# Optimization experiments

Hardware: AMD Instinct MI355X
Metric: run time of the kernel (lower is better)

The kernel has to match this reference:

```python
import jax, jax.numpy as jnp
import numpy as np

B, S, D = 4, 2048, 1024

def setup_inputs() -> dict:
    key = jax.random.key(0)
    kx, kq, kk, kv = jax.random.split(key, 4)
    scale = 0.02
    return {
        'x': jax.random.normal(kx, (B, S, D), dtype=jnp.float32),
        'wq': jax.random.normal(kq, (D, D), dtype=jnp.float32) * scale,
        'wk': jax.random.normal(kk, (D, D), dtype=jnp.float32) * scale,
        'wv': jax.random.normal(kv, (D, D), dtype=jnp.float32) * scale,
    }

def reference(x, wq, wk, wv):
    # QKV projections (no bias): nn.Linear applies x @ W^T; here wq is already [d_in, d_out]
    q = jnp.einsum('bsd,de->bse', x, wq)
    k = jnp.einsum('bsd,de->bse', x, wk)
    v = jnp.einsum('bsd,de->bse', x, wv)
    d_k = k.shape[-1]
    scores = jnp.einsum('bqd,bkd->bqk', q, k) / jnp.sqrt(jnp.float32(d_k))
    s = x.shape[1]
    causal = jnp.tril(jnp.ones((s, s), dtype=bool))  # True = keep
    scores = jnp.where(causal[None, :, :], scores, -jnp.inf)
    attn = jax.nn.softmax(scores, axis=-1)
    # dropout p=0.0 -> identity
    return jnp.einsum('bqk,bkd->bqd', attn, v)
```

## Files before the change

### kernel.cpp

```cpp
#include <hip/hip_runtime.h>
#include <hip/hip_bf16.h>


typedef __attribute__((ext_vector_type(8))) short bf16x8;
typedef __attribute__((ext_vector_type(4))) float f32x4;

#define GLOAD_LDS16(g, l)                                                     \
    __builtin_amdgcn_global_load_lds(                                         \
        (const __attribute__((address_space(1))) void*)(g),                   \
        (__attribute__((address_space(3))) void*)(l), 16, 0, 0)

__device__ __forceinline__ short f2bf(float f) {
    union { float f; unsigned u; } v; v.f = f;
    unsigned r = v.u + 0x7FFFu + ((v.u >> 16) & 1u);
    return (short)(r >> 16);
}
__device__ __forceinline__ float bf2f(short h) {
    union { unsigned u; float f; } v;
    v.u = ((unsigned)(unsigned short)h) << 16;
    return v.f;
}

__global__ __launch_bounds__(256) void convall(
    const float* __restrict__ x, const float* __restrict__ wq,
    const float* __restrict__ wk, short* __restrict__ xb,
    short* __restrict__ wqb, short* __restrict__ wkb) {
    int i = blockIdx.x * 256 + threadIdx.x;
#pragma unroll
    for (int s = 0; s < 5; ++s) {
        int v = i + s * 524288;
        const float* src;
        short* dst;
        int off;
        if (v < 2097152)      { src = x;  dst = xb;  off = v; }
        else if (v < 2359296) { src = wq; dst = wqb; off = v - 2097152; }
        else                  { src = wk; dst = wkb; off = v - 2359296; }
        float4 w = ((const float4*)src)[off];
        short4 o;
        o.x = f2bf(w.x); o.y = f2bf(w.y); o.z = f2bf(w.z); o.w = f2bf(w.w);
        ((short4*)dst)[off] = o;
    }
}

__global__ __launch_bounds__(256) void wtrans(const float* __restrict__ W,
                                              short* __restrict__ O) {
    int n0 = blockIdx.x * 64, k0 = blockIdx.y * 64;
    __shared__ float tile[64][65];
    int t = threadIdx.x;
#pragma unroll
    for (int i = 0; i < 16; ++i) {
        int idx = t + i * 256;
        int r = idx >> 6, c = idx & 63;
        tile[r][c] = W[(size_t)(k0 + r) * 1024 + n0 + c];
    }
    __syncthreads();
#pragma unroll
    for (int i = 0; i < 16; ++i) {
        int idx = t + i * 256;
        int r = idx >> 6, c = idx & 63;
        O[(size_t)(n0 + r) * 1024 + k0 + c] = f2bf(tile[c][r]);
    }
}

template <int MODE>
__global__ __launch_bounds__(256, 3) void gemm128(
    const short* __restrict__ A0, int lda0, long long sA,
    const short* __restrict__ B0, int ldb0, long long sB,
    void* __restrict__ C0, float scale,
    const short* __restrict__ Av, const short* __restrict__ Bv,
    short* __restrict__ Cv) {

    int m0, n0, z = 0, lda = lda0, ldb = ldb0;
    const short* Ab;
    const short* Bb;
    bool isVT = false;

    {
        const int nblk = gridDim.x;
        const int raw = blockIdx.x;
        int bid = (raw & 7) * (nblk >> 3) + (raw >> 3);
        if (MODE == 5) {
            m0 = (bid >> 3) * 128;
            n0 = (bid & 7) * 128;
            Ab = A0; Bb = B0;
        } else {
            if (bid < 544) {
                z = bid / 136;
                int f = bid - z * 136;
                int mt = (int)((sqrtf(8.f * f + 1.f) - 1.f) * 0.5f);
                if (mt * (mt + 1) / 2 > f) --mt;
                if ((mt + 1) * (mt + 2) / 2 <= f) ++mt;
                int nt_ = f - mt * (mt + 1) / 2;
                m0 = mt * 128; n0 = nt_ * 128;
                Ab = A0 + (size_t)z * sA;
                Bb = B0 + (size_t)z * sB;
            } else {
                isVT = true;
                int v = bid - 544;
                m0 = (v >> 6) * 128;
                n0 = (v & 63) * 128;
                Ab = Av; Bb = Bv; lda = 1024; ldb = 1024;
            }
        }
    }

    const int tid = threadIdx.x;
    const int lane = tid & 63;
    const int wid = tid >> 6;
    const int wm = wid >> 1, wn = wid & 1;

    __shared__ __align__(16) short As[3][4096];
    __shared__ __align__(16) short Bs[3][4096];

    f32x4 acc[4][4] = {};

    const int nt = 32;

    const int srow = tid >> 2;
    const int sl = (tid & 3) ^ ((tid >> 3) & 3);
    const short* Agp = Ab + (size_t)(m0 + srow) * lda + sl * 8;
    const short* Bgp = Bb + (size_t)(n0 + srow) * ldb + sl * 8;

#define SA(kt, bf)                                                            \
    do {                                                                      \
        const int _k = (kt) << 5;                                             \
        GLOAD_LDS16(Agp + _k,                    &As[bf][tid * 8]);           \
        GLOAD_LDS16(Agp + _k + (size_t)64 * lda, &As[bf][2048 + tid * 8]);    \
    } while (0)
#define SB(kt, bf)                                                            \
    do {                                                                      \
        const int _k = (kt) << 5;                                             \
        GLOAD_LDS16(Bgp + _k,                    &Bs[bf][tid * 8]);           \
        GLOAD_LDS16(Bgp + _k + (size_t)64 * ldb, &Bs[bf][2048 + tid * 8]);    \
    } while (0)

    const int r = lane & 15;
    const int g = lane >> 4;

#define LDA4(dst, bf)                                                         \
    _Pragma("unroll") for (int q_ = 0; q_ < 4; ++q_) {                        \
        const int rr = wm * 64 + q_ * 16 + r;                                 \
        dst[q_] = *(const bf16x8*)&As[bf][rr * 32 +                           \
                                          ((g ^ ((rr >> 1) & 3))) * 8];       \
    }
#define LDB4(dst, bf)                                                         \
    _Pragma("unroll") for (int q_ = 0; q_ < 4; ++q_) {                        \
        const int rb = wn * 64 + q_ * 16 + r;                                 \
        dst[q_] = *(const bf16x8*)&Bs[bf][rb * 32 +                           \
                                          ((g ^ ((rb >> 1) & 3))) * 8];       \
    }
#define LGKM0()                                                               \
    asm volatile("s_waitcnt lgkmcnt(0)" ::: "memory");                        \
    __builtin_amdgcn_sched_barrier(0)
#define VMC(n) asm volatile("s_waitcnt vmcnt(" #n ")" ::: "memory")
#define BAR() __builtin_amdgcn_s_barrier()
#define MF(ar, br)                                                            \
    _Pragma("unroll") for (int mi = 0; mi < 4; ++mi)                          \
        _Pragma("unroll") for (int ni = 0; ni < 4; ++ni)                      \
            acc[mi][ni] = __builtin_amdgcn_mfma_f32_16x16x32_bf16(            \
                ar[mi], br[ni], acc[mi][ni], 0, 0, 0);

    SA(0, 0); SB(0, 0);
    SA(1, 1); SB(1, 1);

    int bf = 0;
    int bs = 2;
    for (int t = 0; t < nt; ++t) {
        bf16x8 a[4], b[4];
        if (t + 2 < nt) {
            SA(t + 2, bs); SB(t + 2, bs);
            VMC(8);
        } else if (t + 1 < nt) {
            VMC(4);
        } else {
            VMC(0);
        }
        BAR();
        LDA4(a, bf); LDB4(b, bf);
        LGKM0();
        MF(a, b);
        BAR();
        bf = (bf == 2) ? 0 : bf + 1;
        bs = (bs == 2) ? 0 : bs + 1;
    }

    const int r4 = (lane >> 4) * 4;
#pragma unroll
    for (int mi = 0; mi < 4; ++mi) {
#pragma unroll
        for (int ni = 0; ni < 4; ++ni) {
            int col = n0 + wn * 64 + ni * 16 + r;
#pragma unroll
            for (int i = 0; i < 4; ++i) {
                int rr = m0 + wm * 64 + mi * 16 + r4 + i;
                float v = acc[mi][ni][i];
                if (MODE == 5) {
                    ((short*)C0)[(size_t)rr * 1024 + col] = f2bf(v * scale);
                } else {
                    if (isVT) {
                        Cv[(size_t)(col >> 11) * 2097152 +
                           (size_t)rr * 2048 + (col & 2047)] = f2bf(v);
                    } else if (col <= rr) {
                        ((short*)C0)[(size_t)z * 4194304 +
                                     (size_t)rr * 2048 + col] = f2bf(v);
                    }
                }
            }
        }
    }
#undef SA
#undef SB
#undef LDA4
#undef LDB4
#undef LGKM0
#undef VMC
#undef BAR
#undef MF
}

template <int MODE>
__global__ __launch_bounds__(128, 2) void gemm64(
    const short* __restrict__ A0, int lda, long long sA,
    const short* __restrict__ B0, int ldb, long long sB,
    void* __restrict__ C0, float scale) {

    int m0, n0, z = 0;
    const short* Ab;
    const short* Bb;

    if (MODE == 2) {
        int i = blockIdx.x;
        int j = i & 255;
        int mt = j >> 3;
        z = (j >> 1) & 3;
        m0 = mt * 64;
        n0 = ((j & 1) + (i >> 8) * 2) * 128;
        Ab = A0 + (size_t)z * sA;
        Bb = B0 + (size_t)z * sB;
    } else {
        const int nblk = gridDim.x;
        const int raw = blockIdx.x;
        int bid = (raw & 7) * (nblk >> 3) + (raw >> 3);
        m0 = (bid >> 3) * 64;
        n0 = (bid & 7) * 128;
        Ab = A0; Bb = B0;
    }

    const int tid = threadIdx.x;
    const int lane = tid & 63;
    const int wn = tid >> 6;

    __shared__ __align__(16) short As[3][2048];
    __shared__ __align__(16) short Bs[3][4096];

    f32x4 acc[4][4] = {};

    const int Kend = (MODE == 2) ? (((m0 + 63) | 127) + 1) : 1024;
    const int nt = Kend >> 5;

    const int srow = tid >> 2;
    const int sl = (tid & 3) ^ ((tid >> 3) & 3);
    const short* Agp = Ab + (size_t)(m0 + srow) * lda + sl * 8;
    const short* Bgp = Bb + (size_t)(n0 + srow) * ldb + sl * 8;

#define SA6(kt, bf)                                                           \
    do {                                                                      \
        const int _k = (kt) << 5;                                             \
        GLOAD_LDS16(Agp + _k,                    &As[bf][tid * 8]);           \
        GLOAD_LDS16(Agp + _k + (size_t)32 * lda, &As[bf][1024 + tid * 8]);    \
    } while (0)
#define SB6(kt, bf)                                                           \
    do {                                                                      \
        const int _k = (kt) << 5;                                             \
        GLOAD_LDS16(Bgp + _k,                    &Bs[bf][tid * 8]);           \
        GLOAD_LDS16(Bgp + _k + (size_t)32 * ldb, &Bs[bf][1024 + tid * 8]);    \
        GLOAD_LDS16(Bgp + _k + (size_t)64 * ldb, &Bs[bf][2048 + tid * 8]);    \
        GLOAD_LDS16(Bgp + _k + (size_t)96 * ldb, &Bs[bf][3072 + tid * 8]);    \
    } while (0)

    const int r = lane & 15;
    const int g = lane >> 4;

#define LDA4g(dst, bf)                                                        \
    _Pragma("unroll") for (int q_ = 0; q_ < 4; ++q_) {                        \
        const int rr = q_ * 16 + r;                                           \
        dst[q_] = *(const bf16x8*)&As[bf][rr * 32 +                           \
                                          ((g ^ ((rr >> 1) & 3))) * 8];       \
    }
#define LDB4g(dst, bf)                                                        \
    _Pragma("unroll") for (int q_ = 0; q_ < 4; ++q_) {                        \
        const int rb = wn * 64 + q_ * 16 + r;                                 \
        dst[q_] = *(const bf16x8*)&Bs[bf][rb * 32 +                           \
                                          ((g ^ ((rb >> 1) & 3))) * 8];       \
    }
#define LGKM0()                                                               \
    asm volatile("s_waitcnt lgkmcnt(0)" ::: "memory");                        \
    __builtin_amdgcn_sched_barrier(0)
#define VMC(n) asm volatile("s_waitcnt vmcnt(" #n ")" ::: "memory")
#define BAR() __builtin_amdgcn_s_barrier()
#define MF(ar, br)                                                            \
    _Pragma("unroll") for (int mi = 0; mi < 4; ++mi)                          \
        _Pragma("unroll") for (int ni = 0; ni < 4; ++ni)                      \
            acc[mi][ni] = __builtin_amdgcn_mfma_f32_16x16x32_bf16(            \
                ar[mi], br[ni], acc[mi][ni], 0, 0, 0);

    SA6(0, 0); SB6(0, 0);
    SA6(1, 1); SB6(1, 1);

    int bf = 0;
    int bs = 2;
    for (int t = 0; t < nt; ++t) {
        bf16x8 a[4], b[4];
        if (t + 2 < nt) {
            SA6(t + 2, bs); SB6(t + 2, bs);
            VMC(12);
        } else if (t + 1 < nt) {
            VMC(6);
        } else {
            VMC(0);
        }
        BAR();
        LDA4g(a, bf); LDB4g(b, bf);
        LGKM0();
        MF(a, b);
        BAR();
        bf = (bf == 2) ? 0 : bf + 1;
        bs = (bs == 2) ? 0 : bs + 1;
    }

    const int r4 = (lane >> 4) * 4;
#pragma unroll
    for (int mi = 0; mi < 4; ++mi) {
#pragma unroll
        for (int ni = 0; ni < 4; ++ni) {
            int col = n0 + wn * 64 + ni * 16 + r;
#pragma unroll
            for (int i = 0; i < 4; ++i) {
                int rr = m0 + mi * 16 + r4 + i;
                float v = acc[mi][ni][i];
                if (MODE == 0) {
                    ((short*)C0)[(size_t)rr * 1024 + col] = f2bf(v * scale);
                } else {
                    ((float*)C0)[(size_t)z * 2097152 +
                                 (size_t)rr * 1024 + col] = v;
                }
            }
        }
    }
#undef SA6
#undef SB6
#undef LDA4g
#undef LDB4g
#undef LGKM0
#undef VMC
#undef BAR
#undef MF
}

__global__ __launch_bounds__(256) void softmax_wave(short* __restrict__ scores) {
    int row = (blockIdx.x << 2) + (threadIdx.x >> 6);
    int lane = threadIdx.x & 63;
    int b = row >> 11, i = row & 2047;
    short* srow = scores + ((size_t)(b << 11) + i) * 2048;
    int L = i + 1;
    int Lpad = (i | 127) + 1;

    float vals[32];
    float mx = -1e30f;
#pragma unroll
    for (int s = 0; s < 4; ++s) {
        if (s * 512 < Lpad) {
            int j0 = (s << 9) + (lane << 3);
            bf16x8 h = *(const bf16x8*)&srow[j0];
#pragma unroll
            for (int e = 0; e < 8; ++e) {
                float f = ((j0 + e) < L) ? bf2f(h[e]) : -1e30f;
                vals[s * 8 + e] = f;
                mx = fmaxf(mx, f);
            }
        }
    }
#pragma unroll
    for (int o = 32; o > 0; o >>= 1) mx = fmaxf(mx, __shfl_down(mx, o));
    mx = __shfl(mx, 0);

    float sum = 0.f;
#pragma unroll
    for (int s = 0; s < 4; ++s) {
        if (s * 512 < Lpad) {
#pragma unroll
            for (int e = 0; e < 8; ++e) {
                float ex = __expf(vals[s * 8 + e] - mx);
                vals[s * 8 + e] = ex;
                sum += ex;
            }
        }
    }
#pragma unroll
    for (int o = 32; o > 0; o >>= 1) sum += __shfl_down(sum, o);
    sum = __shfl(sum, 0);
    float rinv = 1.0f / sum;

#pragma unroll
    for (int s = 0; s < 4; ++s) {
        if (s * 512 < Lpad) {
            int j0 = (s << 9) + (lane << 3);
            bf16x8 o8;
#pragma unroll
            for (int e = 0; e < 8; ++e) o8[e] = f2bf(vals[s * 8 + e] * rinv);
            *(bf16x8*)&srow[j0] = o8;
        }
    }
}

extern "C" void kernel_launch(void* const* d_in, const int* in_sizes, int n_in,
                              void* d_out, int out_size, void* d_ws, size_t ws_size,
                              hipStream_t stream) {
    const float* x  = (const float*)d_in[0];
    const float* wq = (const float*)d_in[1];
    const float* wk = (const float*)d_in[2];
    const float* wv = (const float*)d_in[3];
    float* out = (float*)d_out;

    short* ws16 = (short*)d_ws;
    short* xb  = ws16;
    short* wqb = xb + 8388608;
    short* wkb = wqb + 1048576;
    short* wtv = wkb + 1048576;
    short* Mt  = wtv + 1048576;
    short* tb  = Mt + 1048576;
    short* vt  = tb + 8388608;
    short* scores = vt + 8388608;

    convall<<<2048, 256, 0, stream>>>(x, wq, wk, xb, wqb, wkb);
    wtrans<<<dim3(16, 16, 1), 256, 0, stream>>>(wv, wtv);
    gemm64<0><<<128, 128, 0, stream>>>(
        wkb, 1024, 0LL, wqb, 1024, 0LL, Mt, 0.03125f);
    gemm128<5><<<512, 256, 0, stream>>>(
        xb, 1024, 0LL, Mt, 1024, 0LL, tb, 1.0f,
        nullptr, nullptr, nullptr);
    gemm128<1><<<1056, 256, 0, stream>>>(
        tb, 1024, 2097152LL, xb, 1024, 2097152LL, scores, 1.0f,
        wtv, xb, vt);
    softmax_wave<<<2048, 256, 0, stream>>>(scores);
    gemm64<2><<<1024, 128, 0, stream>>>(
        scores, 2048, 4194304LL, vt, 2048, 2097152LL, out, 1.0f);
}
```

Baseline: 168.5 us.

## Widen GEMM tiles to 128x256 with double-buffered LDS pipeline

The 128x128 GEMM kernel becomes a 128x256 tile kernel. Each wave now holds 4x8 MFMA accumulators, and the block count for the projection and score/V-transpose launches is halved. The LDS pipeline drops from triple to double buffering, leaving only one stage in flight, and occupancy is lowered to 2 blocks per CU. The aim is more MFMA work per LDS load and less redundant A-tile traffic, at the cost of higher register pressure, less latency hiding and coarser causal tiles that compute more masked-out area.

```diff
diff --git a/kernel.cpp b/kernel.cpp
--- a/kernel.cpp
+++ b/kernel.cpp
@@ -63,14 +63,14 @@
 }
 
 template <int MODE>
-__global__ __launch_bounds__(256, 3) void gemm128(
-    const short* __restrict__ A0, int lda0, long long sA,
-    const short* __restrict__ B0, int ldb0, long long sB,
-    void* __restrict__ C0, float scale,
+__global__ __launch_bounds__(256, 2) void gemm_hw(
+    const short* __restrict__ A0, long long sA,
+    const short* __restrict__ B0, long long sB,
+    void* __restrict__ C0,
     const short* __restrict__ Av, const short* __restrict__ Bv,
     short* __restrict__ Cv) {
 
-    int m0, n0, z = 0, lda = lda0, ldb = ldb0;
+    int m0, n0, z = 0;
     const short* Ab;
     const short* Bb;
     bool isVT = false;
@@ -80,26 +80,29 @@
         const int raw = blockIdx.x;
         int bid = (raw & 7) * (nblk >> 3) + (raw >> 3);
         if (MODE == 5) {
-            m0 = (bid >> 3) * 128;
-            n0 = (bid & 7) * 128;
+            m0 = (bid >> 2) * 128;
+            n0 = (bid & 3) * 256;
             Ab = A0; Bb = B0;
         } else {
-            if (bid < 544) {
-                z = bid / 136;
-                int f = bid - z * 136;
-                int mt = (int)((sqrtf(8.f * f + 1.f) - 1.f) * 0.5f);
-                if (mt * (mt + 1) / 2 > f) --mt;
-                if ((mt + 1) * (mt + 2) / 2 <= f) ++mt;
-                int nt_ = f - mt * (mt + 1) / 2;
-                m0 = mt * 128; n0 = nt_ * 128;
+            if (bid < 288) {
+                z = bid / 72;
+                int f = bid - z * 72;
+                int mt = 0;
+                for (; mt < 16; ++mt) {
+                    int c = (mt >> 1) + 1;
+                    if (f < c) break;
+                    f -= c;
+                }
+                m0 = mt * 128;
+                n0 = f * 256;
                 Ab = A0 + (size_t)z * sA;
                 Bb = B0 + (size_t)z * sB;
             } else {
                 isVT = true;
-                int v = bid - 544;
-                m0 = (v >> 6) * 128;
-                n0 = (v & 63) * 128;
-                Ab = Av; Bb = Bv; lda = 1024; ldb = 1024;
+                int v = bid - 288;
+                m0 = (v >> 5) * 128;
+                n0 = (v & 31) * 256;
+                Ab = Av; Bb = Bv;
             }
         }
     }
@@ -109,29 +112,31 @@
     const int wid = tid >> 6;
     const int wm = wid >> 1, wn = wid & 1;
 
-    __shared__ __align__(16) short As[3][4096];
-    __shared__ __align__(16) short Bs[3][4096];
-
-    f32x4 acc[4][4] = {};
+    __shared__ __align__(16) short As[2][4096];
+    __shared__ __align__(16) short Bs[2][8192];
+
+    f32x4 acc[4][8] = {};
 
     const int nt = 32;
 
     const int srow = tid >> 2;
     const int sl = (tid & 3) ^ ((tid >> 3) & 3);
-    const short* Agp = Ab + (size_t)(m0 + srow) * lda + sl * 8;
-    const short* Bgp = Bb + (size_t)(n0 + srow) * ldb + sl * 8;
+    const short* Agp = Ab + (size_t)(m0 + srow) * 1024 + sl * 8;
+    const short* Bgp = Bb + (size_t)(n0 + srow) * 1024 + sl * 8;
 
 #define SA(kt, bf)                                                            \
     do {                                                                      \
         const int _k = (kt) << 5;                                             \
-        GLOAD_LDS16(Agp + _k,                    &As[bf][tid * 8]);           \
-        GLOAD_LDS16(Agp + _k + (size_t)64 * lda, &As[bf][2048 + tid * 8]);    \
+        GLOAD_LDS16(Agp + _k,            &As[bf][tid * 8]);                   \
+        GLOAD_LDS16(Agp + _k + 65536,    &As[bf][2048 + tid * 8]);            \
     } while (0)
 #define SB(kt, bf)                                                            \
     do {                                                                      \
         const int _k = (kt) << 5;                                             \
-        GLOAD_LDS16(Bgp + _k,                    &Bs[bf][tid * 8]);           \
-        GLOAD_LDS16(Bgp + _k + (size_t)64 * ldb, &Bs[bf][2048 + tid * 8]);    \
+        GLOAD_LDS16(Bgp + _k,            &Bs[bf][tid * 8]);                   \
+        GLOAD_LDS16(Bgp + _k + 65536,    &Bs[bf][2048 + tid * 8]);            \
+        GLOAD_LDS16(Bgp + _k + 131072,   &Bs[bf][4096 + tid * 8]);            \
+        GLOAD_LDS16(Bgp + _k + 196608,   &Bs[bf][6144 + tid * 8]);            \
     } while (0)
 
     const int r = lane & 15;
@@ -143,9 +148,9 @@
         dst[q_] = *(const bf16x8*)&As[bf][rr * 32 +                           \
                                           ((g ^ ((rr >> 1) & 3))) * 8];       \
     }
-#define LDB4(dst, bf)                                                         \
-    _Pragma("unroll") for (int q_ = 0; q_ < 4; ++q_) {                        \
-        const int rb = wn * 64 + q_ * 16 + r;                                 \
+#define LDB8(dst, bf)                                                         \
+    _Pragma("unroll") for (int q_ = 0; q_ < 8; ++q_) {                        \
+        const int rb = wn * 128 + q_ * 16 + r;                                \
         dst[q_] = *(const bf16x8*)&Bs[bf][rb * 32 +                           \
                                           ((g ^ ((rb >> 1) & 3))) * 8];       \
     }
@@ -154,48 +159,44 @@
     __builtin_amdgcn_sched_barrier(0)
 #define VMC(n) asm volatile("s_waitcnt vmcnt(" #n ")" ::: "memory")
 #define BAR() __builtin_amdgcn_s_barrier()
-#define MF(ar, br)                                                            \
-    _Pragma("unroll") for (int mi = 0; mi < 4; ++mi)                          \
-        _Pragma("unroll") for (int ni = 0; ni < 4; ++ni)                      \
-            acc[mi][ni] = __builtin_amdgcn_mfma_f32_16x16x32_bf16(            \
-                ar[mi], br[ni], acc[mi][ni], 0, 0, 0);
 
     SA(0, 0); SB(0, 0);
-    SA(1, 1); SB(1, 1);
-
-    int bf = 0;
-    int bs = 2;
+
+    int buf = 0;
     for (int t = 0; t < nt; ++t) {
-        bf16x8 a[4], b[4];
-        if (t + 2 < nt) {
-            SA(t + 2, bs); SB(t + 2, bs);
-            VMC(8);
-        } else if (t + 1 < nt) {
-            VMC(4);
+        const int nb = buf ^ 1;
+        bf16x8 a[4], b[8];
+        if (t + 1 < nt) {
+            SA(t + 1, nb); SB(t + 1, nb);
+            VMC(6);
         } else {
             VMC(0);
         }
         BAR();
-        LDA4(a, bf); LDB4(b, bf);
+        LDA4(a, buf); LDB8(b, buf);
         LGKM0();
-        MF(a, b);
+#pragma unroll
+        for (int mi = 0; mi < 4; ++mi)
+#pragma unroll
+            for (int ni = 0; ni < 8; ++ni)
+                acc[mi][ni] = __builtin_amdgcn_mfma_f32_16x16x32_bf16(
+                    a[mi], b[ni], acc[mi][ni], 0, 0, 0);
         BAR();
-        bf = (bf == 2) ? 0 : bf + 1;
-        bs = (bs == 2) ? 0 : bs + 1;
+        buf = nb;
     }
 
     const int r4 = (lane >> 4) * 4;
 #pragma unroll
     for (int mi = 0; mi < 4; ++mi) {
 #pragma unroll
-        for (int ni = 0; ni < 4; ++ni) {
-            int col = n0 + wn * 64 + ni * 16 + r;
+        for (int ni = 0; ni < 8; ++ni) {
+            int col = n0 + wn * 128 + ni * 16 + r;
 #pragma unroll
             for (int i = 0; i < 4; ++i) {
                 int rr = m0 + wm * 64 + mi * 16 + r4 + i;
                 float v = acc[mi][ni][i];
                 if (MODE == 5) {
-                    ((short*)C0)[(size_t)rr * 1024 + col] = f2bf(v * scale);
+                    ((short*)C0)[(size_t)rr * 1024 + col] = f2bf(v);
                 } else {
                     if (isVT) {
                         Cv[(size_t)(col >> 11) * 2097152 +
@@ -211,11 +212,10 @@
 #undef SA
 #undef SB
 #undef LDA4
-#undef LDB4
+#undef LDB8
 #undef LGKM0
 #undef VMC
 #undef BAR
-#undef MF
 }
 
 template <int MODE>
@@ -436,12 +436,10 @@
     wtrans<<<dim3(16, 16, 1), 256, 0, stream>>>(wv, wtv);
     gemm64<0><<<128, 128, 0, stream>>>(
         wkb, 1024, 0LL, wqb, 1024, 0LL, Mt, 0.03125f);
-    gemm128<5><<<512, 256, 0, stream>>>(
-        xb, 1024, 0LL, Mt, 1024, 0LL, tb, 1.0f,
-        nullptr, nullptr, nullptr);
-    gemm128<1><<<1056, 256, 0, stream>>>(
-        tb, 1024, 2097152LL, xb, 1024, 2097152LL, scores, 1.0f,
-        wtv, xb, vt);
+    gemm_hw<5><<<256, 256, 0, stream>>>(
+        xb, 0LL, Mt, 0LL, tb, nullptr, nullptr, nullptr);
+    gemm_hw<1><<<544, 256, 0, stream>>>(
+        tb, 2097152LL, xb, 2097152LL, scores, wtv, xb, vt);
     softmax_wave<<<2048, 256, 0, stream>>>(scores);
     gemm64<2><<<1024, 128, 0, stream>>>(
         scores, 2048, 4194304LL, vt, 2048, 2097152LL, out, 1.0f);
```

Measured after the change: 192.6 us. +14.3%, slower.

## Software-pipeline LDS-to-register fragment loads across MFMA in both GEMM kernels

Applied to the files above, without the earlier changes.

Both GEMM main loops are unrolled by two and use ping-pong register fragment sets (aP/bP, aQ/bQ). The LDS reads for the next k-tile are issued before the MFMAs for the current tile, with partial lgkmcnt waits in place of a full drain. This hides LDS read latency behind MFMA work, at the cost of doubling fragment register use. The shape assumes an even tile count, and the occupancy hint of 2 blocks per CU could be at risk.

```diff
diff --git a/kernel.cpp b/kernel.cpp
--- a/kernel.cpp
+++ b/kernel.cpp
@@ -149,8 +149,8 @@
         dst[q_] = *(const bf16x8*)&Bs[bf][rb * 32 +                           \
                                           ((g ^ ((rb >> 1) & 3))) * 8];       \
     }
-#define LGKM0()                                                               \
-    asm volatile("s_waitcnt lgkmcnt(0)" ::: "memory");                        \
+#define LGKM(n)                                                               \
+    asm volatile("s_waitcnt lgkmcnt(" #n ")" ::: "memory");                   \
     __builtin_amdgcn_sched_barrier(0)
 #define VMC(n) asm volatile("s_waitcnt vmcnt(" #n ")" ::: "memory")
 #define BAR() __builtin_amdgcn_s_barrier()
@@ -159,29 +159,39 @@
         _Pragma("unroll") for (int ni = 0; ni < 4; ++ni)                      \
             acc[mi][ni] = __builtin_amdgcn_mfma_f32_16x16x32_bf16(            \
                 ar[mi], br[ni], acc[mi][ni], 0, 0, 0);
+#define SUCC(v) ((v) == 2 ? 0 : (v) + 1)
 
     SA(0, 0); SB(0, 0);
     SA(1, 1); SB(1, 1);
-
-    int bf = 0;
-    int bs = 2;
-    for (int t = 0; t < nt; ++t) {
-        bf16x8 a[4], b[4];
+    VMC(4);
+    BAR();
+    bf16x8 aP[4], bP[4], aQ[4], bQ[4];
+    LDA4(aP, 0); LDB4(bP, 0);
+
+    int bf = 0, bs = 2;
+    for (int t = 0; t < nt; t += 2) {
+        int b1 = SUCC(bf);
+        if (t + 2 < nt) { SA(t + 2, bs); SB(t + 2, bs); bs = SUCC(bs); VMC(4); }
+        else VMC(0);
+        BAR();
+        LDA4(aQ, b1); LDB4(bQ, b1);
+        LGKM(8);
+        MF(aP, bP);
+        BAR();
+        bf = b1;
+        b1 = SUCC(bf);
+        if (t + 3 < nt) { SA(t + 3, bs); SB(t + 3, bs); bs = SUCC(bs); VMC(4); }
+        else if (t + 2 < nt) VMC(0);
+        BAR();
         if (t + 2 < nt) {
-            SA(t + 2, bs); SB(t + 2, bs);
-            VMC(8);
-        } else if (t + 1 < nt) {
-            VMC(4);
+            LDA4(aP, b1); LDB4(bP, b1);
+            LGKM(8);
         } else {
-            VMC(0);
-        }
-        BAR();
-        LDA4(a, bf); LDB4(b, bf);
-        LGKM0();
-        MF(a, b);
-        BAR();
-        bf = (bf == 2) ? 0 : bf + 1;
-        bs = (bs == 2) ? 0 : bs + 1;
+            LGKM(0);
+        }
+        MF(aQ, bQ);
+        BAR();
+        bf = b1;
     }
 
     const int r4 = (lane >> 4) * 4;
@@ -212,10 +222,11 @@
 #undef SB
 #undef LDA4
 #undef LDB4
-#undef LGKM0
+#undef LGKM
 #undef VMC
 #undef BAR
 #undef MF
+#undef SUCC
 }
 
 template <int MODE>
@@ -293,8 +304,8 @@
         dst[q_] = *(const bf16x8*)&Bs[bf][rb * 32 +                           \
                                           ((g ^ ((rb >> 1) & 3))) * 8];       \
     }
-#define LGKM0()                                                               \
-    asm volatile("s_waitcnt lgkmcnt(0)" ::: "memory");                        \
+#define LGKM(n)                                                               \
+    asm volatile("s_waitcnt lgkmcnt(" #n ")" ::: "memory");                   \
     __builtin_amdgcn_sched_barrier(0)
 #define VMC(n) asm volatile("s_waitcnt vmcnt(" #n ")" ::: "memory")
 #define BAR() __builtin_amdgcn_s_barrier()
@@ -303,29 +314,39 @@
         _Pragma("unroll") for (int ni = 0; ni < 4; ++ni)                      \
             acc[mi][ni] = __builtin_amdgcn_mfma_f32_16x16x32_bf16(            \
                 ar[mi], br[ni], acc[mi][ni], 0, 0, 0);
+#define SUCC(v) ((v) == 2 ? 0 : (v) + 1)
 
     SA6(0, 0); SB6(0, 0);
     SA6(1, 1); SB6(1, 1);
-
-    int bf = 0;
-    int bs = 2;
-    for (int t = 0; t < nt; ++t) {
-        bf16x8 a[4], b[4];
+    VMC(6);
+    BAR();
+    bf16x8 aP[4], bP[4], aQ[4], bQ[4];
+    LDA4g(aP, 0); LDB4g(bP, 0);
+
+    int bf = 0, bs = 2;
+    for (int t = 0; t < nt; t += 2) {
+        int b1 = SUCC(bf);
+        if (t + 2 < nt) { SA6(t + 2, bs); SB6(t + 2, bs); bs = SUCC(bs); VMC(6); }
+        else VMC(0);
+        BAR();
+        LDA4g(aQ, b1); LDB4g(bQ, b1);
+        LGKM(8);
+        MF(aP, bP);
+        BAR();
+        bf = b1;
+        b1 = SUCC(bf);
+        if (t + 3 < nt) { SA6(t + 3, bs); SB6(t + 3, bs); bs = SUCC(bs); VMC(6); }
+        else if (t + 2 < nt) VMC(0);
+        BAR();
         if (t + 2 < nt) {
-            SA6(t + 2, bs); SB6(t + 2, bs);
-            VMC(12);
-        } else if (t + 1 < nt) {
-            VMC(6);
+            LDA4g(aP, b1); LDB4g(bP, b1);
+            LGKM(8);
         } else {
-            VMC(0);
-        }
-        BAR();
-        LDA4g(a, bf); LDB4g(b, bf);
-        LGKM0();
-        MF(a, b);
-        BAR();
-        bf = (bf == 2) ? 0 : bf + 1;
-        bs = (bs == 2) ? 0 : bs + 1;
+            LGKM(0);
+        }
+        MF(aQ, bQ);
+        BAR();
+        bf = b1;
     }
 
     const int r4 = (lane >> 4) * 4;
@@ -351,10 +372,11 @@
 #undef SB6
 #undef LDA4g
 #undef LDB4g
-#undef LGKM0
+#undef LGKM
 #undef VMC
 #undef BAR
 #undef MF
+#undef SUCC
 }
 
 __global__ __launch_bounds__(256) void softmax_wave(short* __restrict__ scores) {
```

Measured after the change: 173.7 us. 3.1% more time.
